# Optimization experiments

Measured on AMD Instinct MI355X. Metric: run time of the kernel, lower is better.

Reference implementation:

```python
import jax, jax.numpy as jnp
import numpy as np

N_NODES = 100000
N_EDGES = 1600000
N_GRAPHS = 2048
HID = 64
IN_F = 14
N_CLS = 2
EPS = 1e-5


def _gcn_conv(x, row, col, w_edge, W, b, n_nodes):
    # PyG GCNConv with add_self_loops=True, normalize=True.
    xw = x @ W  # [N, out]
    # degree on target nodes, self-loop contributes weight 1
    deg = jnp.zeros((n_nodes,), x.dtype).at[col].add(w_edge) + 1.0
    dinv = deg ** -0.5
    norm = dinv[row] * w_edge * dinv[col]  # [E]
    out = jnp.zeros_like(xw).at[col].add(norm[:, None] * xw[row])
    out = out + (dinv * dinv)[:, None] * xw  # self-loop term
    return out + b


def _bn_relu(x, gamma, beta):
    mean = jnp.mean(x, axis=0)
    var = jnp.var(x, axis=0)  # biased, as PyTorch BN training normalization
    y = gamma * (x - mean) * jax.lax.rsqrt(var + EPS) + beta
    return jax.nn.relu(y)


def setup_inputs() -> dict:
    key = jax.random.key(0)
    ks = jax.random.split(key, 8)
    x = jax.random.normal(ks[0], (N_NODES, IN_F), dtype=jnp.float32)
    edge_index = jax.random.randint(ks[1], (2, N_EDGES), 0, N_NODES, dtype=jnp.int64)
    batch = jnp.sort(jax.random.randint(ks[2], (N_NODES,), 0, N_GRAPHS, dtype=jnp.int64))
    edge_weight = jnp.ones((N_EDGES,), dtype=jnp.float32)
    def lin(k, fi, fo):
        s = 1.0 / np.sqrt(fi)
        kw, kb = jax.random.split(k)
        return (jax.random.uniform(kw, (fi, fo), jnp.float32, -s, s),
                jax.random.uniform(kb, (fo,), jnp.float32, -s, s))
    W1, b1 = lin(ks[3], IN_F, HID)
    W2, b2 = lin(ks[4], HID, HID)
    W3, b3 = lin(ks[5], HID, HID)
    fcW, fcb = lin(ks[6], HID, N_CLS)
    g = jnp.ones((HID,), jnp.float32)
    z = jnp.zeros((HID,), jnp.float32)
    return {
        "x": x, "edge_index": edge_index, "batch": batch, "edge_weight": edge_weight,
        "W1": W1, "b1": b1, "W2": W2, "b2": b2, "W3": W3, "b3": b3,
        "g1": g, "bt1": z, "g2": g, "bt2": z, "g3": g, "bt3": z,
        "fcW": fcW, "fcb": fcb,
    }


def reference(x, edge_index, batch, edge_weight, W1, b1, W2, b2, W3, b3,
              g1, bt1, g2, bt2, g3, bt3, fcW, fcb):
    row, col = edge_index[0], edge_index[1]
    n = x.shape[0]
    h = _bn_relu(_gcn_conv(x, row, col, edge_weight, W1, b1, n), g1, bt1)
    h = _bn_relu(_gcn_conv(h, row, col, edge_weight, W2, b2, n), g2, bt2)
    h = _bn_relu(_gcn_conv(h, row, col, edge_weight, W3, b3, n), g3, bt3)
    node_embs = h  # dropout p=0 is identity
    graph_emb = jax.ops.segment_sum(node_embs, batch, num_segments=N_GRAPHS)
    out = graph_emb @ fcW + fcb
    return (out, node_embs, graph_emb)
```

## Files before the change

kernel.cpp:

```cpp
#include <hip/hip_runtime.h>

#define N_NODES 100000
#define N_EDGES 1600000
#define N_GRAPHS 2048
#define HID 64
#define IN_F 14
#define N_CLS 2
#define EPS 1e-5f

#define BSHIFT 9
#define NBUCK 196
#define ABLOCKS 256
#define CHUNK (N_EDGES / ABLOCKS)

typedef _Float16 half_t;
typedef _Float16 half8 __attribute__((ext_vector_type(8)));
typedef float f32x4 __attribute__((ext_vector_type(4)));

#define GSTRIDE ((size_t)N_NODES * 16)


__global__ __launch_bounds__(256) void histA_kernel(const int* __restrict__ col,
                                                    int* __restrict__ histG) {
    __shared__ int hl[NBUCK];
    for (int i = threadIdx.x; i < NBUCK; i += 256) hl[i] = 0;
    __syncthreads();
    int e0 = blockIdx.x * CHUNK;
    for (int e = e0 + threadIdx.x; e < e0 + CHUNK; e += 256)
        atomicAdd(&hl[col[e] >> BSHIFT], 1);
    __syncthreads();
    for (int i = threadIdx.x; i < NBUCK; i += 256)
        histG[i * ABLOCKS + blockIdx.x] = hl[i];
}

__global__ __launch_bounds__(256) void scanS1_kernel(const int* __restrict__ histG,
                                                     int* __restrict__ bsumA) {
    __shared__ int ls[256];
    ls[threadIdx.x] = histG[blockIdx.x * 256 + threadIdx.x];
    __syncthreads();
    for (int off = 128; off > 0; off >>= 1) {
        if (threadIdx.x < off) ls[threadIdx.x] += ls[threadIdx.x + off];
        __syncthreads();
    }
    if (threadIdx.x == 0) bsumA[blockIdx.x] = ls[0];
}

__global__ __launch_bounds__(512) void topscan_kernel(int* __restrict__ bsum, int nb) {
    __shared__ int ls[512];
    int t = threadIdx.x;
    int v = (t < nb) ? bsum[t] : 0;
    ls[t] = v;
    __syncthreads();
    for (int off = 1; off < 512; off <<= 1) {
        int x = ls[t];
        if (t >= off) x += ls[t - off];
        __syncthreads();
        ls[t] = x;
        __syncthreads();
    }
    if (t < nb) bsum[t] = ls[t] - v;
}

__global__ __launch_bounds__(256) void scanS3_kernel(int* __restrict__ histG,
                                                     const int* __restrict__ bsumA,
                                                     int* __restrict__ ptr) {
    __shared__ int ls[256];
    int idx = blockIdx.x * 256 + threadIdx.x;
    int v = histG[idx];
    ls[threadIdx.x] = v;
    __syncthreads();
    for (int off = 1; off < 256; off <<= 1) {
        int x = ls[threadIdx.x];
        if (threadIdx.x >= off) x += ls[threadIdx.x - off];
        __syncthreads();
        ls[threadIdx.x] = x;
        __syncthreads();
    }
    histG[idx] = ls[threadIdx.x] - v + bsumA[blockIdx.x];
    if (blockIdx.x == 0 && threadIdx.x == 0) ptr[N_NODES] = N_EDGES;
}

__global__ __launch_bounds__(256) void scatterA_kernel(const int* __restrict__ row,
                                                       const int* __restrict__ col,
                                                       const float* __restrict__ w,
                                                       const int* __restrict__ histG,
                                                       int2* __restrict__ EA) {
    __shared__ int cur[NBUCK];
    for (int i = threadIdx.x; i < NBUCK; i += 256)
        cur[i] = histG[i * ABLOCKS + blockIdx.x];
    __syncthreads();
    int e0 = blockIdx.x * CHUNK;
    for (int e = e0 + threadIdx.x; e < e0 + CHUNK; e += 256) {
        int c = col[e];
        int r = row[e];
        int fx = (int)__float2uint_rn(w[e] * 8192.0f);
        int pos = atomicAdd(&cur[c >> BSHIFT], 1);
        EA[pos] = make_int2(r, (fx << 17) | c);
    }
}

__global__ __launch_bounds__(256) void bucket_kernel(const int2* __restrict__ EA,
                                                     const int* __restrict__ bsumA,
                                                     int2* __restrict__ EB,
                                                     int* __restrict__ ptr,
                                                     float* __restrict__ dinv) {
    __shared__ int hist[512], wsum[512], cur[512];
    int b = blockIdx.x;
    int beg = bsumA[b];
    int end = (b == NBUCK - 1) ? N_EDGES : bsumA[b + 1];
    int i0 = threadIdx.x, i1 = threadIdx.x + 256;
    hist[i0] = 0; hist[i1] = 0;
    wsum[i0] = 0; wsum[i1] = 0;
    __syncthreads();
    for (int e = beg + threadIdx.x; e < end; e += 256) {
        int2 ed = EA[e];
        int c9 = ed.y & 511;
        atomicAdd(&hist[c9], 1);
        atomicAdd(&wsum[c9], (int)((unsigned int)ed.y >> 17));
    }
    __syncthreads();
    int cnt0 = hist[i0], cnt1 = hist[i1];
    for (int off = 1; off < 512; off <<= 1) {
        int v0 = hist[i0], v1 = hist[i1];
        int a0 = (i0 >= off) ? hist[i0 - off] : 0;
        int a1 = (i1 >= off) ? hist[i1 - off] : 0;
        __syncthreads();
        hist[i0] = v0 + a0;
        hist[i1] = v1 + a1;
        __syncthreads();
    }
    int excl0 = hist[i0] - cnt0, excl1 = hist[i1] - cnt1;
    cur[i0] = beg + excl0;
    cur[i1] = beg + excl1;
    int col0 = (b << BSHIFT) + i0, col1 = (b << BSHIFT) + i1;
    if (col0 < N_NODES) {
        ptr[col0] = beg + excl0;
        dinv[col0] = rsqrtf(1.0f + (float)wsum[i0] * (1.0f / 8192.0f));
    }
    if (col1 < N_NODES) {
        ptr[col1] = beg + excl1;
        dinv[col1] = rsqrtf(1.0f + (float)wsum[i1] * (1.0f / 8192.0f));
    }
    __syncthreads();
    for (int e = beg + threadIdx.x; e < end; e += 256) {
        int2 ed = EA[e];
        int pos = atomicAdd(&cur[ed.y & 511], 1);
        EB[pos] = ed;
    }
}

__global__ __launch_bounds__(256) void finalize_kernel(const int2* __restrict__ EB,
                                                       const float* __restrict__ dinv,
                                                       unsigned int* __restrict__ edges, int E) {
    int stride = gridDim.x * blockDim.x;
    for (int e = blockIdx.x * blockDim.x + threadIdx.x; e < E; e += stride) {
        int2 ed = EB[e];
        int c = ed.y & 0x1ffff;
        float w = (float)((unsigned int)ed.y >> 17) * (1.0f / 8192.0f);
        float nrm = dinv[ed.x] * w * dinv[c];
        unsigned int nb = __float_as_uint(nrm);
        unsigned int n15 = (nb + 0x8000u) >> 16;
        if (n15 > 0x7fffu) n15 = 0x7fffu;
        edges[e] = ((unsigned int)ed.x << 15) | n15;
    }
}


template <int K>
__global__ __launch_bounds__(256) void gemm_kernel(const float* __restrict__ h,
                                                   const float* __restrict__ W,
                                                   half_t* __restrict__ xw, int n_nodes) {
    int f = threadIdx.x & 63;
    float wcol[K];
#pragma unroll
    for (int k = 0; k < K; k++) wcol[k] = W[k * HID + f];
    half_t* xg = xw + (size_t)(f >> 4) * GSTRIDE + (f & 15);
    int wave = (blockIdx.x * blockDim.x + threadIdx.x) >> 6;
    int nwaves = (gridDim.x * blockDim.x) >> 6;
    for (int n = wave; n < n_nodes; n += nwaves) {
        const float* hr = h + (size_t)n * K;
        float acc = 0.f;
#pragma unroll
        for (int k = 0; k < K; k++) acc += hr[k] * wcol[k];
        xg[(size_t)n * 16] = (half_t)acc;
    }
}

__global__ __launch_bounds__(256) void gemm_bn_mfma_kernel(const float* __restrict__ h,
                                                           const float* __restrict__ W,
                                                           const float* __restrict__ stats,
                                                           const float* __restrict__ gamma,
                                                           const float* __restrict__ beta,
                                                           half_t* __restrict__ xw, int n_nodes) {
    __shared__ float sc_s[HID], sh_s[HID];
    if (threadIdx.x < 64) {
        float mean = stats[threadIdx.x] * (1.0f / N_NODES);
        float var = stats[64 + threadIdx.x] * (1.0f / N_NODES) - mean * mean;
        float sc = gamma[threadIdx.x] * rsqrtf(var + EPS);
        sc_s[threadIdx.x] = sc;
        sh_s[threadIdx.x] = beta[threadIdx.x] - mean * sc;
    }
    __syncthreads();
    int lane = threadIdx.x & 63;
    int col16 = lane & 15;
    int quad = lane >> 4;

    float scA[2][8], shA[2][8];
#pragma unroll
    for (int kh = 0; kh < 2; kh++)
#pragma unroll
        for (int j = 0; j < 8; j++) {
            int k = kh * 32 + quad * 8 + j;
            scA[kh][j] = sc_s[k];
            shA[kh][j] = sh_s[k];
        }

    half8 bfrag[4][2];
#pragma unroll
    for (int t = 0; t < 4; t++)
#pragma unroll
        for (int kh = 0; kh < 2; kh++)
#pragma unroll
            for (int j = 0; j < 8; j++) {
                int k = kh * 32 + quad * 8 + j;
                bfrag[t][kh][j] = (half_t)W[k * HID + t * 16 + col16];
            }

    int wave = (blockIdx.x * blockDim.x + threadIdx.x) >> 6;
    int nwaves = (gridDim.x * blockDim.x) >> 6;
    int ntiles = n_nodes >> 4;
    for (int tIdx = wave; tIdx < ntiles; tIdx += nwaves) {
        int n0 = tIdx << 4;
        const float* hr = h + (size_t)(n0 + col16) * HID + quad * 8;
        half8 afrag[2];
#pragma unroll
        for (int kh = 0; kh < 2; kh++) {
            float4 p0 = *(const float4*)(hr + kh * 32);
            float4 p1 = *(const float4*)(hr + kh * 32 + 4);
            float fv[8] = {p0.x, p0.y, p0.z, p0.w, p1.x, p1.y, p1.z, p1.w};
#pragma unroll
            for (int j = 0; j < 8; j++) {
                float v = fv[j] * scA[kh][j] + shA[kh][j];
                afrag[kh][j] = (half_t)fmaxf(v, 0.f);
            }
        }
        f32x4 acc[4];
#pragma unroll
        for (int t = 0; t < 4; t++) {
            f32x4 z = {0.f, 0.f, 0.f, 0.f};
            acc[t] = __builtin_amdgcn_mfma_f32_16x16x32_f16(afrag[0], bfrag[t][0], z, 0, 0, 0);
            acc[t] = __builtin_amdgcn_mfma_f32_16x16x32_f16(afrag[1], bfrag[t][1], acc[t], 0, 0, 0);
        }
#pragma unroll
        for (int t = 0; t < 4; t++) {
            half_t* xg = xw + (size_t)t * GSTRIDE;
#pragma unroll
            for (int r = 0; r < 4; r++) {
                int rowi = n0 + quad * 4 + r;
                xg[(size_t)rowi * 16 + col16] = (half_t)acc[t][r];
            }
        }
    }
}

__global__ __launch_bounds__(256) void gather_stats_kernel(const int* __restrict__ ptr,
                                                           const unsigned int* __restrict__ edges,
                                                           const half_t* __restrict__ xw,
                                                           const float* __restrict__ dinv,
                                                           const float* __restrict__ b,
                                                           float* __restrict__ h,
                                                           float* __restrict__ stats,
                                                           int n_nodes) {
    int g = (blockIdx.x & 7) >> 1;
    int grank = ((blockIdx.x >> 3) << 1) | (blockIdx.x & 1);
    int lane16 = threadIdx.x & 15;
    int quadLocal = threadIdx.x >> 4;
    int quadId = grank * 16 + quadLocal;
    int nquads = (gridDim.x >> 2) * 16;

    const half_t* xg = xw + (size_t)g * GSTRIDE;
    const char* xgb = (const char*)xg + lane16 * 2;
    int f = g * 16 + lane16;
    float bf = b[f];
    int base = ((threadIdx.x & 63) >> 4) * 16;

    float s = 0.f, s2 = 0.f;
    for (int n = quadId; n < n_nodes; n += nquads) {
        int beg = ptr[n];
        int c = ptr[n + 1] - beg;
        float a0 = 0.f, a1 = 0.f, a2 = 0.f, a3 = 0.f;
        for (int j0 = 0; j0 < c; j0 += 16) {
            int m = c - j0;
            if (m > 16) m = 16;
            int ev = 0;
            if (lane16 < m) ev = (int)edges[beg + j0 + lane16];
            int j = 0;
            for (; j + 4 <= m; j += 4) {
                unsigned int u0 = (unsigned int)__shfl(ev, base + j);
                unsigned int u1 = (unsigned int)__shfl(ev, base + j + 1);
                unsigned int u2 = (unsigned int)__shfl(ev, base + j + 2);
                unsigned int u3 = (unsigned int)__shfl(ev, base + j + 3);
                float w0 = __uint_as_float((u0 & 0x7fffu) << 16);
                float w1 = __uint_as_float((u1 & 0x7fffu) << 16);
                float w2 = __uint_as_float((u2 & 0x7fffu) << 16);
                float w3 = __uint_as_float((u3 & 0x7fffu) << 16);
                float x0 = (float)*(const half_t*)(xgb + ((size_t)(u0 >> 15) << 5));
                float x1 = (float)*(const half_t*)(xgb + ((size_t)(u1 >> 15) << 5));
                float x2 = (float)*(const half_t*)(xgb + ((size_t)(u2 >> 15) << 5));
                float x3 = (float)*(const half_t*)(xgb + ((size_t)(u3 >> 15) << 5));
                a0 += w0 * x0; a1 += w1 * x1; a2 += w2 * x2; a3 += w3 * x3;
            }
            if (j < m) {
                unsigned int u = (unsigned int)__shfl(ev, base + j);
                a1 += __uint_as_float((u & 0x7fffu) << 16) *
                      (float)*(const half_t*)(xgb + ((size_t)(u >> 15) << 5));
            }
            if (j + 1 < m) {
                unsigned int u = (unsigned int)__shfl(ev, base + j + 1);
                a2 += __uint_as_float((u & 0x7fffu) << 16) *
                      (float)*(const half_t*)(xgb + ((size_t)(u >> 15) << 5));
            }
            if (j + 2 < m) {
                unsigned int u = (unsigned int)__shfl(ev, base + j + 2);
                a3 += __uint_as_float((u & 0x7fffu) << 16) *
                      (float)*(const half_t*)(xgb + ((size_t)(u >> 15) << 5));
            }
        }
        float di = dinv[n];
        float v = ((a0 + a1) + (a2 + a3)) + di * di * (float)xg[(size_t)n * 16 + lane16] + bf;
        h[(size_t)n * HID + f] = v;
        s += v;
        s2 += v * v;
    }
    __shared__ float ls[256], ls2[256];
    ls[threadIdx.x] = s;
    ls2[threadIdx.x] = s2;
    __syncthreads();
    if (threadIdx.x < 16) {
        float a = 0.f, aa = 0.f;
#pragma unroll
        for (int k = 0; k < 16; k++) {
            a += ls[k * 16 + threadIdx.x];
            aa += ls2[k * 16 + threadIdx.x];
        }
        atomicAdd(&stats[g * 16 + threadIdx.x], a);
        atomicAdd(&stats[64 + g * 16 + threadIdx.x], aa);
    }
}

__global__ __launch_bounds__(256) void bn_relu_seg_kernel(float* __restrict__ h,
                                                          const float* __restrict__ stats,
                                                          const float* __restrict__ gamma,
                                                          const float* __restrict__ beta,
                                                          const int* __restrict__ batch,
                                                          float* __restrict__ gemb,
                                                          int n_nodes) {
    int g = blockIdx.x * blockDim.x + threadIdx.x;
    int f = g & 63;
    int wave = g >> 6;
    int nwaves = (gridDim.x * blockDim.x) >> 6;
    int chunk = (n_nodes + nwaves - 1) / nwaves;
    int n0 = wave * chunk;
    int n1 = n0 + chunk;
    if (n1 > n_nodes) n1 = n_nodes;
    if (n0 >= n_nodes) return;
    float mean = stats[f] * (1.0f / N_NODES);
    float var = stats[64 + f] * (1.0f / N_NODES) - mean * mean;
    float sc = gamma[f] * rsqrtf(var + EPS);
    float sh = beta[f] - mean * sc;
    int curg = batch[n0];
    float racc = 0.f;
    for (int n = n0; n < n1; n++) {
        int bg = batch[n];
        if (bg != curg) {
            atomicAdd(&gemb[(size_t)curg * HID + f], racc);
            racc = 0.f;
            curg = bg;
        }
        size_t idx = (size_t)n * HID + f;
        float v = h[idx] * sc + sh;
        v = fmaxf(v, 0.f);
        h[idx] = v;
        racc += v;
    }
    atomicAdd(&gemb[(size_t)curg * HID + f], racc);
}

__global__ __launch_bounds__(256) void final_kernel(const float* __restrict__ gemb,
                                                    const float* __restrict__ fcW,
                                                    const float* __restrict__ fcb,
                                                    float* __restrict__ out) {
    int g = blockIdx.x * blockDim.x + threadIdx.x;
    if (g >= N_GRAPHS * N_CLS) return;
    int gr = g >> 1, c = g & 1;
    float acc = fcb[c];
#pragma unroll
    for (int k = 0; k < HID; k++) acc += gemb[gr * HID + k] * fcW[k * N_CLS + c];
    out[g] = acc;
}


extern "C" void kernel_launch(void* const* d_in, const int* in_sizes, int n_in,
                              void* d_out, int out_size, void* d_ws, size_t ws_size,
                              hipStream_t stream) {
    const float* x    = (const float*)d_in[0];
    const int*   ei   = (const int*)d_in[1];
    const int*   batch= (const int*)d_in[2];
    const float* ew   = (const float*)d_in[3];
    const float* W1   = (const float*)d_in[4];
    const float* b1   = (const float*)d_in[5];
    const float* W2   = (const float*)d_in[6];
    const float* b2   = (const float*)d_in[7];
    const float* W3   = (const float*)d_in[8];
    const float* b3   = (const float*)d_in[9];
    const float* g1   = (const float*)d_in[10];
    const float* bt1  = (const float*)d_in[11];
    const float* g2   = (const float*)d_in[12];
    const float* bt2  = (const float*)d_in[13];
    const float* g3   = (const float*)d_in[14];
    const float* bt3  = (const float*)d_in[15];
    const float* fcW  = (const float*)d_in[16];
    const float* fcb  = (const float*)d_in[17];

    const int* row = ei;
    const int* col = ei + N_EDGES;

    float* out_head  = (float*)d_out;
    float* node_embs = out_head + N_GRAPHS * N_CLS;
    float* gemb      = node_embs + (size_t)N_NODES * HID;

    char* base = (char*)d_ws;
    half_t* xwh = (half_t*)base;
    int2*   EB  = (int2*)base;
    char* r1 = base + (size_t)N_NODES * HID * 2;
    int2*   EA  = (int2*)r1;
    unsigned int* edges = (unsigned int*)r1;
    char* r2 = r1 + (size_t)N_EDGES * 8;
    float* dinv  = (float*)r2;
    float* stats = dinv + N_NODES;
    int*   ptr   = (int*)(stats + 128);
    int*   histG = ptr + N_NODES + 1;
    int*   bsumA = histG + NBUCK * ABLOCKS;

    const int B   = 256;
    const int gGS = 1024;
    const int gGA = 2048;

    histA_kernel<<<ABLOCKS, B, 0, stream>>>(col, histG);
    scanS1_kernel<<<NBUCK, B, 0, stream>>>(histG, bsumA);
    topscan_kernel<<<1, 512, 0, stream>>>(bsumA, NBUCK);
    scanS3_kernel<<<NBUCK, B, 0, stream>>>(histG, bsumA, ptr);
    scatterA_kernel<<<ABLOCKS, B, 0, stream>>>(row, col, ew, histG, EA);
    bucket_kernel<<<NBUCK, B, 0, stream>>>(EA, bsumA, EB, ptr, dinv);
    finalize_kernel<<<gGS, B, 0, stream>>>(EB, dinv, edges, N_EDGES);

    float* h = node_embs;

    gemm_kernel<IN_F><<<gGS, B, 0, stream>>>(x, W1, xwh, N_NODES);
    hipMemsetAsync(stats, 0, 128 * sizeof(float), stream);
    gather_stats_kernel<<<gGA, B, 0, stream>>>(ptr, edges, xwh, dinv, b1, h, stats, N_NODES);

    gemm_bn_mfma_kernel<<<gGS, B, 0, stream>>>(h, W2, stats, g1, bt1, xwh, N_NODES);
    hipMemsetAsync(stats, 0, 128 * sizeof(float), stream);
    gather_stats_kernel<<<gGA, B, 0, stream>>>(ptr, edges, xwh, dinv, b2, h, stats, N_NODES);

    gemm_bn_mfma_kernel<<<gGS, B, 0, stream>>>(h, W3, stats, g2, bt2, xwh, N_NODES);
    hipMemsetAsync(stats, 0, 128 * sizeof(float), stream);
    gather_stats_kernel<<<gGA, B, 0, stream>>>(ptr, edges, xwh, dinv, b3, h, stats, N_NODES);

    hipMemsetAsync(gemb, 0, (size_t)N_GRAPHS * HID * sizeof(float), stream);
    bn_relu_seg_kernel<<<gGS, B, 0, stream>>>(h, stats, g3, bt3, batch, gemb, N_NODES);

    final_kernel<<<(N_GRAPHS * N_CLS + B - 1) / B, B, 0, stream>>>(gemb, fcW, fcb, out_head);
}
```

Measured before the change: 440.4 us.

## Sort nodes by degree for balanced gather and store intermediate activations as fp16

Adds a counting sort of nodes by in-degree that produces a permutation, a permuted CSR pointer array, and edges relocated so each node's edges sit in degree-sorted order. The gather kernel walks nodes in that order, so quads in a wave handle nodes of similar degree and spend less time idle on divergent loop trip counts. Layers 1 and 2 now write their outputs as fp16 in the grouped xw layout, and the MFMA GEMM reads that directly, halving intermediate traffic. The cost is five extra small preprocessing kernels, a scattered write pattern in finalize, and lower precision for the intermediate activations.

```diff
diff --git a/kernel.cpp b/kernel.cpp
--- a/kernel.cpp
+++ b/kernel.cpp
@@ -12,6 +12,9 @@
 #define NBUCK 196
 #define ABLOCKS 256
 #define CHUNK (N_EDGES / ABLOCKS)
+
+#define NBLK2 128
+#define NCHUNK2 ((N_NODES + NBLK2 - 1) / NBLK2)
 
 typedef _Float16 half_t;
 typedef _Float16 half8 __attribute__((ext_vector_type(8)));
@@ -149,8 +152,104 @@
     }
 }
 
+
+__global__ __launch_bounds__(256) void histD_kernel(const int* __restrict__ ptr,
+                                                    int* __restrict__ histD) {
+    __shared__ int hl[2048];
+    for (int i = threadIdx.x; i < 2048; i += 256) hl[i] = 0;
+    __syncthreads();
+    int n0 = blockIdx.x * NCHUNK2;
+    int n1 = n0 + NCHUNK2; if (n1 > N_NODES) n1 = N_NODES;
+    for (int n = n0 + threadIdx.x; n < n1; n += 256) {
+        int d = ptr[n + 1] - ptr[n];
+        if (d > 255) d = 255;
+        atomicAdd(&hl[((threadIdx.x & 7) << 8) + d], 1);
+    }
+    __syncthreads();
+    int s = 0;
+#pragma unroll
+    for (int c = 0; c < 8; c++) s += hl[(c << 8) + threadIdx.x];
+    histD[threadIdx.x * NBLK2 + blockIdx.x] = s;
+}
+
+__global__ __launch_bounds__(128) void scanD1_kernel(const int* __restrict__ histD,
+                                                     int* __restrict__ rowTot) {
+    __shared__ int ls[128];
+    ls[threadIdx.x] = histD[blockIdx.x * NBLK2 + threadIdx.x];
+    __syncthreads();
+    for (int off = 64; off > 0; off >>= 1) {
+        if (threadIdx.x < off) ls[threadIdx.x] += ls[threadIdx.x + off];
+        __syncthreads();
+    }
+    if (threadIdx.x == 0) rowTot[blockIdx.x] = ls[0];
+}
+
+__global__ __launch_bounds__(256) void topscanD_kernel(const int* __restrict__ rowTot,
+                                                       int* __restrict__ nodeExcl,
+                                                       int* __restrict__ edgeExcl,
+                                                       int* __restrict__ ptrS) {
+    __shared__ int a[256], b[256];
+    int t = threadIdx.x;
+    int cnt = rowTot[t];
+    int ec = cnt * t;
+    a[t] = cnt; b[t] = ec;
+    __syncthreads();
+    for (int off = 1; off < 256; off <<= 1) {
+        int va = a[t], vb = b[t];
+        if (t >= off) { va += a[t - off]; vb += b[t - off]; }
+        __syncthreads();
+        a[t] = va; b[t] = vb;
+        __syncthreads();
+    }
+    nodeExcl[t] = a[t] - cnt;
+    edgeExcl[t] = b[t] - ec;
+    if (t == 0) ptrS[N_NODES] = N_EDGES;
+}
+
+__global__ __launch_bounds__(128) void scanD3_kernel(int* __restrict__ histD,
+                                                     const int* __restrict__ nodeExcl) {
+    __shared__ int ls[128];
+    int idx = blockIdx.x * NBLK2 + threadIdx.x;
+    int v = histD[idx];
+    ls[threadIdx.x] = v;
+    __syncthreads();
+    for (int off = 1; off < 128; off <<= 1) {
+        int x = ls[threadIdx.x];
+        if (threadIdx.x >= off) x += ls[threadIdx.x - off];
+        __syncthreads();
+        ls[threadIdx.x] = x;
+        __syncthreads();
+    }
+    histD[idx] = ls[threadIdx.x] - v + nodeExcl[blockIdx.x];
+}
+
+__global__ __launch_bounds__(256) void scatterD_kernel(const int* __restrict__ ptr,
+                                                       const int* __restrict__ histD,
+                                                       const int* __restrict__ nodeExcl,
+                                                       const int* __restrict__ edgeExcl,
+                                                       int* __restrict__ perm,
+                                                       int* __restrict__ ptrS,
+                                                       int* __restrict__ newbase) {
+    __shared__ int cur[256];
+    cur[threadIdx.x] = histD[threadIdx.x * NBLK2 + blockIdx.x];
+    __syncthreads();
+    int n0 = blockIdx.x * NCHUNK2;
+    int n1 = n0 + NCHUNK2; if (n1 > N_NODES) n1 = N_NODES;
+    for (int n = n0 + threadIdx.x; n < n1; n += 256) {
+        int d = ptr[n + 1] - ptr[n];
+        if (d > 255) d = 255;
+        int pos = atomicAdd(&cur[d], 1);
+        int ebase = edgeExcl[d] + (pos - nodeExcl[d]) * d;
+        perm[pos] = n;
+        ptrS[pos] = ebase;
+        newbase[n] = ebase;
+    }
+}
+
 __global__ __launch_bounds__(256) void finalize_kernel(const int2* __restrict__ EB,
                                                        const float* __restrict__ dinv,
+                                                       const int* __restrict__ ptr,
+                                                       const int* __restrict__ newbase,
                                                        unsigned int* __restrict__ edges, int E) {
     int stride = gridDim.x * blockDim.x;
     for (int e = blockIdx.x * blockDim.x + threadIdx.x; e < E; e += stride) {
@@ -161,7 +260,8 @@
         unsigned int nb = __float_as_uint(nrm);
         unsigned int n15 = (nb + 0x8000u) >> 16;
         if (n15 > 0x7fffu) n15 = 0x7fffu;
-        edges[e] = ((unsigned int)ed.x << 15) | n15;
+        int newpos = newbase[c] + (e - ptr[c]);
+        edges[newpos] = ((unsigned int)ed.x << 15) | n15;
     }
 }
 
@@ -186,7 +286,7 @@
     }
 }
 
-__global__ __launch_bounds__(256) void gemm_bn_mfma_kernel(const float* __restrict__ h,
+__global__ __launch_bounds__(256) void gemm_bn_mfma_kernel(const half_t* __restrict__ h,
                                                            const float* __restrict__ W,
                                                            const float* __restrict__ stats,
                                                            const float* __restrict__ gamma,
@@ -231,16 +331,16 @@
     int ntiles = n_nodes >> 4;
     for (int tIdx = wave; tIdx < ntiles; tIdx += nwaves) {
         int n0 = tIdx << 4;
-        const float* hr = h + (size_t)(n0 + col16) * HID + quad * 8;
         half8 afrag[2];
 #pragma unroll
         for (int kh = 0; kh < 2; kh++) {
-            float4 p0 = *(const float4*)(hr + kh * 32);
-            float4 p1 = *(const float4*)(hr + kh * 32 + 4);
-            float fv[8] = {p0.x, p0.y, p0.z, p0.w, p1.x, p1.y, p1.z, p1.w};
+            int k0 = kh * 32 + quad * 8;
+            const half_t* hp = h + (size_t)(k0 >> 4) * GSTRIDE
+                                 + (size_t)(n0 + col16) * 16 + (k0 & 15);
+            half8 raw = *(const half8*)hp;
 #pragma unroll
             for (int j = 0; j < 8; j++) {
-                float v = fv[j] * scA[kh][j] + shA[kh][j];
+                float v = (float)raw[j] * scA[kh][j] + shA[kh][j];
                 afrag[kh][j] = (half_t)fmaxf(v, 0.f);
             }
         }
@@ -263,12 +363,15 @@
     }
 }
 
-__global__ __launch_bounds__(256) void gather_stats_kernel(const int* __restrict__ ptr,
+template <bool LAST>
+__global__ __launch_bounds__(256) void gather_stats_kernel(const int* __restrict__ ptrS,
+                                                           const int* __restrict__ perm,
                                                            const unsigned int* __restrict__ edges,
                                                            const half_t* __restrict__ xw,
                                                            const float* __restrict__ dinv,
                                                            const float* __restrict__ b,
-                                                           float* __restrict__ h,
+                                                           half_t* __restrict__ hp,
+                                                           float* __restrict__ hf,
                                                            float* __restrict__ stats,
                                                            int n_nodes) {
     int g = (blockIdx.x & 7) >> 1;
@@ -280,14 +383,16 @@
 
     const half_t* xg = xw + (size_t)g * GSTRIDE;
     const char* xgb = (const char*)xg + lane16 * 2;
+    half_t* hpg = hp + (size_t)g * GSTRIDE;
     int f = g * 16 + lane16;
     float bf = b[f];
     int base = ((threadIdx.x & 63) >> 4) * 16;
 
     float s = 0.f, s2 = 0.f;
-    for (int n = quadId; n < n_nodes; n += nquads) {
-        int beg = ptr[n];
-        int c = ptr[n + 1] - beg;
+    for (int i = quadId; i < n_nodes; i += nquads) {
+        int node = perm[i];
+        int beg = ptrS[i];
+        int c = ptrS[i + 1] - beg;
         float a0 = 0.f, a1 = 0.f, a2 = 0.f, a3 = 0.f;
         for (int j0 = 0; j0 < c; j0 += 16) {
             int m = c - j0;
@@ -326,9 +431,13 @@
                       (float)*(const half_t*)(xgb + ((size_t)(u >> 15) << 5));
             }
         }
-        float di = dinv[n];
-        float v = ((a0 + a1) + (a2 + a3)) + di * di * (float)xg[(size_t)n * 16 + lane16] + bf;
-        h[(size_t)n * HID + f] = v;
+        float di = dinv[node];
+        float v = ((a0 + a1) + (a2 + a3))
+                  + di * di * (float)xg[(size_t)node * 16 + lane16] + bf;
+        if (LAST)
+            hf[(size_t)node * HID + f] = v;
+        else
+            hpg[(size_t)node * 16 + lane16] = (half_t)v;
         s += v;
         s2 += v * v;
     }
@@ -429,18 +538,27 @@
     float* node_embs = out_head + N_GRAPHS * N_CLS;
     float* gemb      = node_embs + (size_t)N_NODES * HID;
 
-    char* base = (char*)d_ws;
-    half_t* xwh = (half_t*)base;
-    int2*   EB  = (int2*)base;
-    char* r1 = base + (size_t)N_NODES * HID * 2;
+    char* bse = (char*)d_ws;
+    half_t* xwh = (half_t*)bse;
+    int2*   EB  = (int2*)bse;
+    char* r1 = bse + (size_t)N_NODES * HID * 2;
     int2*   EA  = (int2*)r1;
-    unsigned int* edges = (unsigned int*)r1;
-    char* r2 = r1 + (size_t)N_EDGES * 8;
-    float* dinv  = (float*)r2;
+    half_t* hpl = (half_t*)r1;
+    char* r2 = r1 + (size_t)N_NODES * HID * 2;
+    unsigned int* edges = (unsigned int*)r2;
+    char* r3 = r2 + (size_t)N_EDGES * 4;
+    float* dinv  = (float*)r3;
     float* stats = dinv + N_NODES;
     int*   ptr   = (int*)(stats + 128);
     int*   histG = ptr + N_NODES + 1;
     int*   bsumA = histG + NBUCK * ABLOCKS;
+    int*   histD = bsumA + NBUCK + 4;
+    int*   rowTot = histD + 256 * NBLK2;
+    int*   nodeExcl = rowTot + 256;
+    int*   edgeExcl = nodeExcl + 256;
+    int*   perm   = edgeExcl + 256;
+    int*   newbase= perm + N_NODES;
+    int*   ptrS   = newbase + N_NODES;
 
     const int B   = 256;
     const int gGS = 1024;
@@ -452,24 +570,34 @@
     scanS3_kernel<<<NBUCK, B, 0, stream>>>(histG, bsumA, ptr);
     scatterA_kernel<<<ABLOCKS, B, 0, stream>>>(row, col, ew, histG, EA);
     bucket_kernel<<<NBUCK, B, 0, stream>>>(EA, bsumA, EB, ptr, dinv);
-    finalize_kernel<<<gGS, B, 0, stream>>>(EB, dinv, edges, N_EDGES);
-
-    float* h = node_embs;
+
+    histD_kernel<<<NBLK2, B, 0, stream>>>(ptr, histD);
+    scanD1_kernel<<<256, 128, 0, stream>>>(histD, rowTot);
+    topscanD_kernel<<<1, 256, 0, stream>>>(rowTot, nodeExcl, edgeExcl, ptrS);
+    scanD3_kernel<<<256, 128, 0, stream>>>(histD, nodeExcl);
+    scatterD_kernel<<<NBLK2, B, 0, stream>>>(ptr, histD, nodeExcl, edgeExcl,
+                                             perm, ptrS, newbase);
+    finalize_kernel<<<gGS, B, 0, stream>>>(EB, dinv, ptr, newbase, edges, N_EDGES);
+
+    float* h3 = node_embs;
 
     gemm_kernel<IN_F><<<gGS, B, 0, stream>>>(x, W1, xwh, N_NODES);
     hipMemsetAsync(stats, 0, 128 * sizeof(float), stream);
-    gather_stats_kernel<<<gGA, B, 0, stream>>>(ptr, edges, xwh, dinv, b1, h, stats, N_NODES);
-
-    gemm_bn_mfma_kernel<<<gGS, B, 0, stream>>>(h, W2, stats, g1, bt1, xwh, N_NODES);
+    gather_stats_kernel<false><<<gGA, B, 0, stream>>>(ptrS, perm, edges, xwh, dinv,
+                                                      b1, hpl, h3, stats, N_NODES);
+
+    gemm_bn_mfma_kernel<<<gGS, B, 0, stream>>>(hpl, W2, stats, g1, bt1, xwh, N_NODES);
     hipMemsetAsync(stats, 0, 128 * sizeof(float), stream);
-    gather_stats_kernel<<<gGA, B, 0, stream>>>(ptr, edges, xwh, dinv, b2, h, stats, N_NODES);
-
-    gemm_bn_mfma_kernel<<<gGS, B, 0, stream>>>(h, W3, stats, g2, bt2, xwh, N_NODES);
+    gather_stats_kernel<false><<<gGA, B, 0, stream>>>(ptrS, perm, edges, xwh, dinv,
+                                                      b2, hpl, h3, stats, N_NODES);
+
+    gemm_bn_mfma_kernel<<<gGS, B, 0, stream>>>(hpl, W3, stats, g2, bt2, xwh, N_NODES);
     hipMemsetAsync(stats, 0, 128 * sizeof(float), stream);
-    gather_stats_kernel<<<gGA, B, 0, stream>>>(ptr, edges, xwh, dinv, b3, h, stats, N_NODES);
+    gather_stats_kernel<true><<<gGA, B, 0, stream>>>(ptrS, perm, edges, xwh, dinv,
+                                                     b3, hpl, h3, stats, N_NODES);
 
     hipMemsetAsync(gemb, 0, (size_t)N_GRAPHS * HID * sizeof(float), stream);
-    bn_relu_seg_kernel<<<gGS, B, 0, stream>>>(h, stats, g3, bt3, batch, gemb, N_NODES);
+    bn_relu_seg_kernel<<<gGS, B, 0, stream>>>(h3, stats, g3, bt3, batch, gemb, N_NODES);
 
     final_kernel<<<(N_GRAPHS * N_CLS + B - 1) / B, B, 0, stream>>>(gemb, fcW, fcb, out_head);
 }
```

After: 418.4 us. 5.0% less time.
